# Performance work log

Hardware: AMD Instinct MI355X
Metric: run time of the kernel (lower is better)

The kernel has to match this reference:

```python
import jax, jax.numpy as jnp
import numpy as np

C_S = 384; C_Z = 128; C_RES = 128; H = 12; HD = 32; L = 8; RB = 2; NA = 7
TSF = 10.0; EPS = 1e-8; B = 2; N = 512; NRES = 21


def layernorm(x, g, b, eps=1e-5):
    m = jnp.mean(x, -1, keepdims=True)
    v = jnp.mean((x - m) ** 2, -1, keepdims=True)
    return (x - m) * jax.lax.rsqrt(v + eps) * g + b


def lin(x, w, b=None):
    y = x @ w.T
    return y if b is None else y + b


def rot_vec(R, v):
    return jnp.einsum('...ij,...j->...i', R, v)


def make_rigid(n, ca, c, eps=1e-7):
    # Gram-Schmidt backbone frame construction (openfold make_transform_from_reference)
    t = -ca
    n_xyz = n + t; c_xyz = c + t
    cx, cy, cz = c_xyz[..., 0], c_xyz[..., 1], c_xyz[..., 2]
    z = jnp.zeros_like(cx); o = jnp.ones_like(cx)
    nrm = jnp.sqrt(eps + cx**2 + cy**2)
    s1 = -cy / nrm; c1 = cx / nrm
    R1 = jnp.stack([jnp.stack([c1, -s1, z], -1), jnp.stack([s1, c1, z], -1), jnp.stack([z, z, o], -1)], -2)
    nrm2 = jnp.sqrt(eps + cx**2 + cy**2 + cz**2)
    s2 = cz / nrm2; c2 = jnp.sqrt(cx**2 + cy**2) / nrm2
    R2 = jnp.stack([jnp.stack([c2, z, s2], -1), jnp.stack([z, o, z], -1), jnp.stack([-s2, z, c2], -1)], -2)
    Rc = R2 @ R1
    n2 = rot_vec(Rc, n_xyz)
    ny, nz = n2[..., 1], n2[..., 2]
    nrm3 = jnp.sqrt(eps + ny**2 + nz**2)
    sn = -nz / nrm3; cn = ny / nrm3
    Rn = jnp.stack([jnp.stack([o, z, z], -1), jnp.stack([z, cn, -sn], -1), jnp.stack([z, sn, cn], -1)], -2)
    R = jnp.swapaxes(Rn @ Rc, -1, -2)
    return R, ca


def to4x4(R, t):
    bot = jnp.zeros(R.shape[:-2] + (1, 4), R.dtype).at[..., 0, 3].set(1.0)
    top = jnp.concatenate([R, t[..., None]], -1)
    return jnp.concatenate([top, bot], -2)


def compose(R1, t1, R2, t2):
    return R1 @ R2, rot_vec(R1, t2) + t1


def structure_fwd(s, z, aatype, mask, ln_s_g, ln_s_b, ln_z_g, ln_z_b, w_in, b_in, w_b, b_b,
                  attn_ln_g, attn_ln_b, attn_wqkv, attn_wo, attn_bo, attn_wg, attn_bg,
                  tr_ln_g, tr_ln_b, tr_w1, tr_b1, tr_w2, tr_b2, w_bb, b_bb,
                  ar_win, ar_bin, ar_winit, ar_binit, ar_w1, ar_b1, ar_w2, ar_b2, ar_wout, ar_bout,
                  default_frames, group_idx, atom_mask, lit_positions):
    Bd, Nd = s.shape[:2]
    s = layernorm(s, ln_s_g, ln_s_b)
    s_init = s
    s = lin(s, w_in, b_in)
    zn = layernorm(z, ln_z_g, ln_z_b)
    bmat = lin(zn, w_b, b_b)                                # [B,N,N,L*H]
    bmat = jnp.transpose(bmat, (0, 3, 1, 2)).reshape(Bd, L, H, Nd, Nd)
    key_mask = (mask[:, None, None, :] == 0)
    for i in range(L):
        xn = layernorm(s, attn_ln_g[i], attn_ln_b[i])
        t = lin(xn, attn_wqkv[i]).reshape(Bd, Nd, H, 3 * HD).transpose(0, 2, 1, 3)
        q, k, v = jnp.split(t, 3, axis=-1)                  # each [B,H,N,HD]
        a = jnp.einsum('bhqc,bhkc->bhqk', q * HD ** -0.5, k) + bmat[:, i]
        a = jnp.where(key_mask, -1e9, a)
        a = jax.nn.softmax(a, axis=-1)
        y = jnp.einsum('bhqk,bhkc->bqhc', a, v).reshape(Bd, Nd, C_S)
        g = jax.nn.sigmoid(lin(xn, attn_wg[i], attn_bg[i]))
        s = s + lin(g * y, attn_wo[i], attn_bo[i])
        xt = layernorm(s, tr_ln_g[i], tr_ln_b[i])
        s = s + lin(jax.nn.relu(lin(xt, tr_w1[i], tr_b1[i])), tr_w2[i], tr_b2[i])
    # angle resnet
    a0 = lin(jax.nn.relu(s_init), ar_winit, ar_binit)
    a = lin(jax.nn.relu(s), ar_win, ar_bin) + a0
    for j in range(RB):
        h = lin(jax.nn.relu(a), ar_w1[j], ar_b1[j])
        h = lin(jax.nn.relu(h), ar_w2[j], ar_b2[j])
        a = a + h
    ang = lin(jax.nn.relu(a), ar_wout, ar_bout).reshape(Bd, Nd, NA, 2)
    unnorm = ang
    denom = jnp.sqrt(jnp.maximum(jnp.sum(ang ** 2, -1, keepdims=True), EPS))
    angles = ang / denom
    # backbone rigid from predicted pseudo-atoms
    n_, ca_, c_ = jnp.split(lin(s, w_bb, b_bb), 3, axis=-1)
    Rbb, tbb = make_rigid(n_, ca_, c_)
    tbb = tbb * TSF
    # torsion_angles_to_frames
    d4 = default_frames[aatype]                             # [B,N,8,4,4]
    dR = d4[..., :3, :3]; dt = d4[..., :3, 3]
    bb_sin = jnp.zeros(angles.shape[:-2] + (1,), angles.dtype)
    bb_cos = jnp.ones_like(bb_sin)
    sin_a = jnp.concatenate([bb_sin, angles[..., 0]], -1)   # [B,N,8]
    cos_a = jnp.concatenate([bb_cos, angles[..., 1]], -1)
    z8 = jnp.zeros_like(sin_a); o8 = jnp.ones_like(sin_a)
    Ra = jnp.stack([jnp.stack([o8, z8, z8], -1), jnp.stack([z8, cos_a, -sin_a], -1), jnp.stack([z8, sin_a, cos_a], -1)], -2)
    Rf = dR @ Ra; tf = dt
    R5, t5 = compose(Rf[..., 4, :, :], tf[..., 4, :], Rf[..., 5, :, :], tf[..., 5, :])
    R6, t6 = compose(R5, t5, Rf[..., 6, :, :], tf[..., 6, :])
    R7, t7 = compose(R6, t6, Rf[..., 7, :, :], tf[..., 7, :])
    Rall = jnp.concatenate([Rf[..., :5, :, :], jnp.stack([R5, R6, R7], -3)], -3)
    tall = jnp.concatenate([tf[..., :5, :], jnp.stack([t5, t6, t7], -2)], -2)
    Rg = jnp.einsum('bnij,bngjk->bngik', Rbb, Rall)
    tg = jnp.einsum('bnij,bngj->bngi', Rbb, tall) + tbb[..., None, :]
    # frames + literature positions -> atom14
    oh = jax.nn.one_hot(group_idx[aatype], 8, dtype=Rg.dtype)   # [B,N,14,8]
    Ratom = jnp.einsum('bnag,bngij->bnaij', oh, Rg)
    tatom = jnp.einsum('bnag,bngi->bnai', oh, tg)
    lit = lit_positions[aatype]                             # [B,N,14,3]
    pred = jnp.einsum('bnaij,bnaj->bnai', Ratom, lit) + tatom
    pred = pred * atom_mask[aatype][..., None]
    return angles, unnorm, to4x4(Rbb, tbb), to4x4(Rg, tg), pred, s


def setup_inputs():
    key = jax.random.key(0)
    ks = iter(jax.random.split(key, 64))
    nrm = lambda shape: jax.random.normal(next(ks), shape, jnp.float32) * 0.02
    d = {}
    d['s'] = jax.random.normal(next(ks), (B, N, C_S), jnp.float32)
    d['z'] = jax.random.normal(next(ks), (B, N, N, C_Z), jnp.float32)
    d['aatype'] = jax.random.randint(next(ks), (B, N), 0, NRES)
    d['mask'] = jax.random.randint(next(ks), (B, N), 0, 2).astype(jnp.int32)
    d['ln_s_g'] = jnp.ones(C_S); d['ln_s_b'] = jnp.zeros(C_S)
    d['ln_z_g'] = jnp.ones(C_Z); d['ln_z_b'] = jnp.zeros(C_Z)
    d['w_in'] = nrm((C_S, C_S)); d['b_in'] = jnp.zeros(C_S)
    d['w_b'] = nrm((L * H, C_Z)); d['b_b'] = jnp.zeros(L * H)
    d['attn_ln_g'] = jnp.ones((L, C_S)); d['attn_ln_b'] = jnp.zeros((L, C_S))
    d['attn_wqkv'] = nrm((L, 3 * C_S, C_S))
    d['attn_wo'] = nrm((L, C_S, C_S)); d['attn_bo'] = jnp.zeros((L, C_S))
    d['attn_wg'] = nrm((L, C_S, C_S)); d['attn_bg'] = jnp.ones((L, C_S))
    d['tr_ln_g'] = jnp.ones((L, C_S)); d['tr_ln_b'] = jnp.zeros((L, C_S))
    d['tr_w1'] = nrm((L, C_S, C_S)); d['tr_b1'] = jnp.zeros((L, C_S))
    d['tr_w2'] = nrm((L, C_S, C_S)); d['tr_b2'] = jnp.zeros((L, C_S))
    d['w_bb'] = nrm((9, C_S)); d['b_bb'] = jnp.zeros(9)
    d['ar_win'] = nrm((C_RES, C_S)); d['ar_bin'] = jnp.zeros(C_RES)
    d['ar_winit'] = nrm((C_RES, C_S)); d['ar_binit'] = jnp.zeros(C_RES)
    d['ar_w1'] = nrm((RB, C_RES, C_RES)); d['ar_b1'] = jnp.zeros((RB, C_RES))
    d['ar_w2'] = nrm((RB, C_RES, C_RES)); d['ar_b2'] = jnp.zeros((RB, C_RES))
    d['ar_wout'] = nrm((2 * NA, C_RES)); d['ar_bout'] = jnp.zeros(2 * NA)
    df = jnp.tile(jnp.eye(4, dtype=jnp.float32), (NRES, 8, 1, 1))
    df = df.at[..., :3, 3].set(jax.random.normal(next(ks), (NRES, 8, 3)))
    d['default_frames'] = df
    d['group_idx'] = jax.random.randint(next(ks), (NRES, 14), 0, 8)
    d['atom_mask'] = (jax.random.uniform(next(ks), (NRES, 14)) < 0.9).astype(jnp.float32)
    d['lit_positions'] = jax.random.normal(next(ks), (NRES, 14, 3), jnp.float32)
    return d


def reference(s, z, aatype, mask, ln_s_g, ln_s_b, ln_z_g, ln_z_b, w_in, b_in, w_b, b_b,
              attn_ln_g, attn_ln_b, attn_wqkv, attn_wo, attn_bo, attn_wg, attn_bg,
              tr_ln_g, tr_ln_b, tr_w1, tr_b1, tr_w2, tr_b2, w_bb, b_bb,
              ar_win, ar_bin, ar_winit, ar_binit, ar_w1, ar_b1, ar_w2, ar_b2, ar_wout, ar_bout,
              default_frames, group_idx, atom_mask, lit_positions):
    return structure_fwd(s, z, aatype, mask, ln_s_g, ln_s_b, ln_z_g, ln_z_b, w_in, b_in, w_b, b_b,
                         attn_ln_g, attn_ln_b, attn_wqkv, attn_wo, attn_bo, attn_wg, attn_bg,
                         tr_ln_g, tr_ln_b, tr_w1, tr_b1, tr_w2, tr_b2, w_bb, b_bb,
                         ar_win, ar_bin, ar_winit, ar_binit, ar_w1, ar_b1, ar_w2, ar_b2, ar_wout, ar_bout,
                         default_frames, group_idx, atom_mask, lit_positions)
```

## Files before the change

### kernel.cpp

```cpp
#include <hip/hip_runtime.h>
#include <hip/hip_bf16.h>

typedef __attribute__((ext_vector_type(8))) short bf16x8;
typedef __attribute__((ext_vector_type(4))) float f32x4;
typedef unsigned short u16;

__device__ __forceinline__ u16 f2bf(float f) {
  union { __hip_bfloat16 b; u16 u; } v;
  v.b = __float2bfloat16(f);
  return v.u;
}
__device__ __forceinline__ float bf2f(u16 s) {
  union { unsigned u; float f; } v; v.u = ((unsigned)s) << 16;
  return v.f;
}
__device__ __forceinline__ f32x4 mfma_bf16(bf16x8 a, bf16x8 b, f32x4 c) {
  return __builtin_amdgcn_mfma_f32_16x16x32_bf16(a, b, c, 0, 0, 0);
}
__device__ __forceinline__ void split2(float x, u16& h, u16& l) {
  h = f2bf(x);
  l = f2bf(x - bf2f(h));
}
template <int SPL>
__device__ __forceinline__ void splitN(float x, u16* o) {
// ... 8 lines not shown
struct P2 { const float* s; u16* d; int n; };
struct Prep2Args { P2 j[7]; };
__global__ __launch_bounds__(256) void prep2_kernel(Prep2Args A, int total4) {
  for (int i4 = blockIdx.x * 256 + threadIdx.x; i4 < total4; i4 += gridDim.x * 256) {
    int i = i4 * 4;
    #pragma unroll
    for (int jj = 0; jj < 7; jj++) {
      if (i < A.j[jj].n) {
        const float* src = A.j[jj].s;
        u16* dh = A.j[jj].d;
        u16* dl = dh + A.j[jj].n;
        float4 v = *(const float4*)(src + i);
        ushort4 h, l;
        split2(v.x, h.x, l.x); split2(v.y, h.y, l.y);
        split2(v.z, h.z, l.z); split2(v.w, h.w, l.w);
        *(ushort4*)(dh + i) = h;
        *(ushort4*)(dl + i) = l;
        break;
      }
      i -= A.j[jj].n;
    }
  }
}
struct P3 { const float* s; u16* d; int n; };
struct Prep3Args { P3 j[4]; };
__global__ __launch_bounds__(256) void prep3_kernel(Prep3Args A, int total4) {
  for (int i4 = blockIdx.x * 256 + threadIdx.x; i4 < total4; i4 += gridDim.x * 256) {
    int i = i4 * 4;
    #pragma unroll
    for (int jj = 0; jj < 4; jj++) {
      if (i < A.j[jj].n) {
        const float* src = A.j[jj].s;
        u16* d0 = A.j[jj].d;
        u16* d1 = d0 + A.j[jj].n;
        u16* d2 = d1 + A.j[jj].n;
        float4 v = *(const float4*)(src + i);
        float xv[4] = {v.x, v.y, v.z, v.w};
        ushort4 o0, o1, o2;
        u16* po0 = (u16*)&o0; u16* po1 = (u16*)&o1; u16* po2 = (u16*)&o2;
        #pragma unroll
        for (int e = 0; e < 4; e++) {
          u16 tmp[3]; splitN<3>(xv[e], tmp);
          po0[e] = tmp[0]; po1[e] = tmp[1]; po2[e] = tmp[2];
        }
        *(ushort4*)(d0 + i) = o0;
        *(ushort4*)(d1 + i) = o1;
        *(ushort4*)(d2 + i) = o2;
        break;
      }
      i -= A.j[jj].n;
    }
  }
}

__global__ __launch_bounds__(256) void ln_kernel(
    const float* __restrict__ x, const float* __restrict__ gamma,
    const float* __restrict__ beta, float* __restrict__ o, int rows, int C) {
  int wid = threadIdx.x >> 6, lane = threadIdx.x & 63;
  int row = blockIdx.x * 4 + wid;
  if (row >= rows) return;
  const float* xr = x + (size_t)row * C;
  float s = 0.f, s2 = 0.f;
  for (int c = lane; c < C; c += 64) { float v = xr[c]; s += v; s2 += v * v; }
  #pragma unroll
  for (int off = 32; off >= 1; off >>= 1) {
    s += __shfl_xor(s, off);
    s2 += __shfl_xor(s2, off);
  }
  float m = s / C;
  float var = s2 / C - m * m;
  float rs = rsqrtf(var + 1e-5f);
  float* orow = o + (size_t)row * C;
  for (int c = lane; c < C; c += 64) orow[c] = (xr[c] - m) * rs * gamma[c] + beta[c];
}

template <int SPL, int LNA, int INRELU, int ACT, int ACC, int STATS, int OUT2>
__global__ __launch_bounds__(128) void gemm_kernel(
    const float* __restrict__ A, const float* __restrict__ pin,
    const float* __restrict__ lng, const float* __restrict__ lnb,
    const u16* __restrict__ w0p, const u16* __restrict__ w1p, const u16* __restrict__ w2p,
    const float* __restrict__ bias,
    float* __restrict__ O, float* __restrict__ O2, float* __restrict__ pout,
    int M, int N, int K) {
  __shared__ __align__(16) u16 a_pl[SPL][32][40];
  __shared__ __align__(16) u16 w_pl[SPL][64][40];
  const int n0 = blockIdx.x * 64, m0 = blockIdx.y * 32;
  const int t = threadIdx.x;
  const int wid = t >> 6, lane = t & 63;
  const int cl = lane & 15, cg = lane >> 4;
  const int ar = t >> 2, aq = t & 3;
  const int wr = t >> 1, wh2 = t & 1;
  const float* ap = A + (size_t)(m0 + ar) * K + aq * 8;
  const u16* wp[SPL];
  {
    const u16* tmp[3] = {w0p, w1p, w2p};
    #pragma unroll
    for (int p = 0; p < SPL; p++) wp[p] = tmp[p] + (size_t)(n0 + wr) * K + wh2 * 16;
  }
  float rm = 0.f, rrs = 1.f;
  if (LNA) {
    float s = 0.f, s2 = 0.f;
    #pragma unroll
    for (int pq = 0; pq < 6; pq++) {
      s  += pin[(m0 + ar) * 16 + pq * 2];
      s2 += pin[(m0 + ar) * 16 + pq * 2 + 1];
    }
    rm = s * (1.f / 384.f);
    rrs = rsqrtf(s2 * (1.f / 384.f) - rm * rm + 1e-5f);
  }
  float4 ra0, ra1, rg0, rg1, rb0, rb1;
  uint4 rw[SPL][2];
  auto GLOAD = [&](int k0) {
    ra0 = ((const float4*)(ap + k0))[0];
    ra1 = ((const float4*)(ap + k0))[1];
    #pragma unroll
    for (int p = 0; p < SPL; p++) {
      rw[p][0] = *(const uint4*)(wp[p] + k0);
      rw[p][1] = *(const uint4*)(wp[p] + k0 + 8);
    }
    if (LNA) {
      rg0 = ((const float4*)(lng + k0 + aq * 8))[0];
      rg1 = ((const float4*)(lng + k0 + aq * 8))[1];
      rb0 = ((const float4*)(lnb + k0 + aq * 8))[0];
      rb1 = ((const float4*)(lnb + k0 + aq * 8))[1];
    }
  };
  GLOAD(0);
  f32x4 acc[4] = {};
  for (int k0 = 0; k0 < K; k0 += 32) {
    {
      float av[8] = {ra0.x, ra0.y, ra0.z, ra0.w, ra1.x, ra1.y, ra1.z, ra1.w};
      if (LNA) {
        float gv[8] = {rg0.x, rg0.y, rg0.z, rg0.w, rg1.x, rg1.y, rg1.z, rg1.w};
        float bv[8] = {rb0.x, rb0.y, rb0.z, rb0.w, rb1.x, rb1.y, rb1.z, rb1.w};
        #pragma unroll
        for (int j = 0; j < 8; j++) av[j] = (av[j] - rm) * rrs * gv[j] + bv[j];
      }
      if (INRELU) {
        #pragma unroll
        for (int j = 0; j < 8; j++) av[j] = fmaxf(av[j], 0.f);
      }
      union { u16 s[8]; uint4 u; } pk[SPL];
      #pragma unroll
      for (int j = 0; j < 8; j++) {
        u16 tmp[SPL]; splitN<SPL>(av[j], tmp);
        #pragma unroll
        for (int p = 0; p < SPL; p++) pk[p].s[j] = tmp[p];
      }
      #pragma unroll
      for (int p = 0; p < SPL; p++) *(uint4*)&a_pl[p][ar][aq * 8] = pk[p].u;
      #pragma unroll
      for (int p = 0; p < SPL; p++) {
        *(uint4*)&w_pl[p][wr][wh2 * 16] = rw[p][0];
        *(uint4*)&w_pl[p][wr][wh2 * 16 + 8] = rw[p][1];
      }
    }
    __syncthreads();
    if (k0 + 32 < K) GLOAD(k0 + 32);
    bf16x8 av[SPL];
    #pragma unroll
    for (int p = 0; p < SPL; p++) av[p] = *(const bf16x8*)&a_pl[p][wid * 16 + cl][cg * 8];
    bf16x8 bv[SPL][4];
    #pragma unroll
    for (int p = 0; p < SPL; p++)
      #pragma unroll
      for (int nt = 0; nt < 4; nt++)
        bv[p][nt] = *(const bf16x8*)&w_pl[p][nt * 16 + cl][cg * 8];
    #pragma unroll
    for (int d = 0; d < SPL; d++)
      #pragma unroll
      for (int i2 = 0; i2 <= d; i2++) {
        #pragma unroll
        for (int nt = 0; nt < 4; nt++)
          acc[nt] = mfma_bf16(av[i2], bv[d - i2][nt], acc[nt]);
      }
    __syncthreads();
  }
  float ps[4], ps2[4];
  #pragma unroll
  for (int i = 0; i < 4; i++) { ps[i] = 0.f; ps2[i] = 0.f; }
  #pragma unroll
  for (int nt = 0; nt < 4; nt++) {
    #pragma unroll
    for (int i = 0; i < 4; i++) {
      int r = m0 + wid * 16 + cg * 4 + i;
      int c = n0 + nt * 16 + cl;
      float v = acc[nt][i];
      if (bias) v += bias[c];
      if (ACT == 1) v = fmaxf(v, 0.f);
      if (ACT == 2) v = 1.f / (1.f + __expf(-v));
      size_t oi = (size_t)r * N + c;
      float nv = ACC ? (O[oi] + v) : v;
      O[oi] = nv;
      if (OUT2) O2[oi] = nv;
      if (STATS) { ps[i] += nv; ps2[i] += nv * nv; }
    }
  }
  if (STATS) {
    #pragma unroll
    for (int i = 0; i < 4; i++) {
      #pragma unroll
      for (int off = 1; off < 16; off <<= 1) {
        ps[i] += __shfl_xor(ps[i], off);
        ps2[i] += __shfl_xor(ps2[i], off);
      }
    }
    if (cl == 0) {
      #pragma unroll
      for (int i = 0; i < 4; i++) {
        int r = m0 + wid * 16 + cg * 4 + i;
        pout[r * 16 + blockIdx.x * 2] = ps[i];
        pout[r * 16 + blockIdx.x * 2 + 1] = ps2[i];
      }
    }
  }
}

__global__ __launch_bounds__(128) void gemm_qkvg_kernel(
    const float* __restrict__ A, const float* __restrict__ pin,
    const float* __restrict__ lng, const float* __restrict__ lnb,
    const u16* __restrict__ wqh, const u16* __restrict__ wql,
    const u16* __restrict__ wgh, const u16* __restrict__ wgl,
    const float* __restrict__ bg,
    u16* __restrict__ qkvh, u16* __restrict__ qkvl, float* __restrict__ gbuf) {
  __shared__ __align__(16) u16 a_pl[2][32][40];
  __shared__ __align__(16) u16 w_pl[2][64][40];
  const int n0 = blockIdx.x * 64, m0 = blockIdx.y * 32;
  const bool isg = (n0 >= 1152);
  const int t = threadIdx.x;
  const int wid = t >> 6, lane = t & 63;
  const int cl = lane & 15, cg = lane >> 4;
  const int ar = t >> 2, aq = t & 3;
  const int wr = t >> 1, wh2 = t & 1;
  const float* ap = A + (size_t)(m0 + ar) * 384 + aq * 8;
  const u16* wph = (isg ? wgh + (size_t)(n0 - 1152 + wr) * 384 : wqh + (size_t)(n0 + wr) * 384) + wh2 * 16;
  const u16* wpl = (isg ? wgl + (size_t)(n0 - 1152 + wr) * 384 : wql + (size_t)(n0 + wr) * 384) + wh2 * 16;
  float s = 0.f, s2 = 0.f;
  #pragma unroll
  for (int pq = 0; pq < 6; pq++) {
    s  += pin[(m0 + ar) * 16 + pq * 2];
    s2 += pin[(m0 + ar) * 16 + pq * 2 + 1];
  }
  const float rm = s * (1.f / 384.f);
  const float rrs = rsqrtf(s2 * (1.f / 384.f) - rm * rm + 1e-5f);
  float4 ra0, ra1, rg0, rg1, rb0, rb1;
  uint4 rwh0, rwh1, rwl0, rwl1;
  auto GLOAD = [&](int k0) {
    ra0 = ((const float4*)(ap + k0))[0];
    ra1 = ((const float4*)(ap + k0))[1];
    rwh0 = *(const uint4*)(wph + k0);
    rwh1 = *(const uint4*)(wph + k0 + 8);
    rwl0 = *(const uint4*)(wpl + k0);
    rwl1 = *(const uint4*)(wpl + k0 + 8);
    rg0 = ((const float4*)(lng + k0 + aq * 8))[0];
    rg1 = ((const float4*)(lng + k0 + aq * 8))[1];
    rb0 = ((const float4*)(lnb + k0 + aq * 8))[0];
    rb1 = ((const float4*)(lnb + k0 + aq * 8))[1];
  };
  GLOAD(0);
  f32x4 acc[4] = {};
  for (int k0 = 0; k0 < 384; k0 += 32) {
    {
      float av[8] = {ra0.x, ra0.y, ra0.z, ra0.w, ra1.x, ra1.y, ra1.z, ra1.w};
      float gv[8] = {rg0.x, rg0.y, rg0.z, rg0.w, rg1.x, rg1.y, rg1.z, rg1.w};
      float bv[8] = {rb0.x, rb0.y, rb0.z, rb0.w, rb1.x, rb1.y, rb1.z, rb1.w};
      union { u16 s[8]; uint4 u; } ph, pl;
      #pragma unroll
      for (int j = 0; j < 8; j++) {
        float x = (av[j] - rm) * rrs * gv[j] + bv[j];
        split2(x, ph.s[j], pl.s[j]);
      }
      *(uint4*)&a_pl[0][ar][aq * 8] = ph.u;
      *(uint4*)&a_pl[1][ar][aq * 8] = pl.u;
      *(uint4*)&w_pl[0][wr][wh2 * 16] = rwh0;
      *(uint4*)&w_pl[0][wr][wh2 * 16 + 8] = rwh1;
      *(uint4*)&w_pl[1][wr][wh2 * 16] = rwl0;
      *(uint4*)&w_pl[1][wr][wh2 * 16 + 8] = rwl1;
    }
    __syncthreads();
    if (k0 + 32 < 384) GLOAD(k0 + 32);
    bf16x8 ah = *(const bf16x8*)&a_pl[0][wid * 16 + cl][cg * 8];
    bf16x8 al = *(const bf16x8*)&a_pl[1][wid * 16 + cl][cg * 8];
    bf16x8 bh[4], bl[4];
    #pragma unroll
    for (int nt = 0; nt < 4; nt++) {
      bh[nt] = *(const bf16x8*)&w_pl[0][nt * 16 + cl][cg * 8];
      bl[nt] = *(const bf16x8*)&w_pl[1][nt * 16 + cl][cg * 8];
    }
    #pragma unroll
    for (int nt = 0; nt < 4; nt++) acc[nt] = mfma_bf16(ah, bh[nt], acc[nt]);
    #pragma unroll
    for (int nt = 0; nt < 4; nt++) acc[nt] = mfma_bf16(ah, bl[nt], acc[nt]);
    #pragma unroll
    for (int nt = 0; nt < 4; nt++) acc[nt] = mfma_bf16(al, bh[nt], acc[nt]);
    __syncthreads();
  }
  #pragma unroll
  for (int nt = 0; nt < 4; nt++) {
    #pragma unroll
    for (int i = 0; i < 4; i++) {
      int r = m0 + wid * 16 + cg * 4 + i;
      int c = n0 + nt * 16 + cl;
      float v = acc[nt][i];
      if (isg) {
        int cc = c - 1152;
        v = 1.f / (1.f + __expf(-(v + bg[cc])));
        gbuf[(size_t)r * 384 + cc] = v;
      } else {
        u16 hh, ll; split2(v, hh, ll);
        qkvh[(size_t)r * 1152 + c] = hh;
        qkvl[(size_t)r * 1152 + c] = ll;
      }
    }
  }
}

__global__ __launch_bounds__(512) void zbmat_kernel(
    const float* __restrict__ z, const float* __restrict__ gamma,
    const float* __restrict__ beta, const u16* __restrict__ wbh,
    const u16* __restrict__ wbl, const float* __restrict__ bbias,
    float* __restrict__ bm) {
  __shared__ __align__(16) u16 w_h[96][136], w_l[96][136];
  __shared__ __align__(16) u16 a_h[2][64][136], a_l[2][64][136];
  const int b = blockIdx.x >> 9;
  const int i = blockIdx.x & 511;
  const int t = threadIdx.x;
  for (int idx = t; idx < 1536; idx += 512) {
    int r2 = idx >> 4, c2 = (idx & 15) * 8;
    *(uint4*)&w_h[r2][c2] = *(const uint4*)(wbh + r2 * 128 + c2);
    *(uint4*)&w_l[r2][c2] = *(const uint4*)(wbl + r2 * 128 + c2);
  }
  const int r = t >> 3, q = t & 7;
  const int cq = q * 16;
  const float* zbase = z + ((size_t)(b * 512 + i) * 512) * 128 + (size_t)r * 128 + cq;
  float4 gv[4], bv[4];
  #pragma unroll
  for (int ii = 0; ii < 4; ii++) {
    gv[ii] = *(const float4*)(gamma + cq + ii * 4);
    bv[ii] = *(const float4*)(beta + cq + ii * 4);
  }
  const int wid = t >> 6, lane = t & 63;
  const int cl = lane & 15, cg = lane >> 4;
  const int m = wid & 3, g = wid >> 2;
  const int arow = m * 16 + cl;
  float bb[3];
  #pragma unroll
  for (int nt = 0; nt < 3; nt++) bb[nt] = bbias[(g * 3 + nt) * 16 + cl];
  float4 v[4];

  auto ln_store = [&](int dst) {
    float s = 0.f, s2 = 0.f;
    #pragma unroll
    for (int ii = 0; ii < 4; ii++) {
      s += v[ii].x + v[ii].y + v[ii].z + v[ii].w;
      s2 += v[ii].x * v[ii].x + v[ii].y * v[ii].y + v[ii].z * v[ii].z + v[ii].w * v[ii].w;
    }
    s += __shfl_xor(s, 1); s2 += __shfl_xor(s2, 1);
    s += __shfl_xor(s, 2); s2 += __shfl_xor(s2, 2);
    s += __shfl_xor(s, 4); s2 += __shfl_xor(s2, 4);
    const float mu = s * (1.f / 128.f);
    const float var = s2 * (1.f / 128.f) - mu * mu;
    const float rs = rsqrtf(var + 1e-5f);
    float xv[16];
    #pragma unroll
    for (int w2 = 0; w2 < 4; w2++) {
      float4 x = v[w2], g2 = gv[w2], be = bv[w2];
      xv[w2 * 4 + 0] = (x.x - mu) * rs * g2.x + be.x;
      xv[w2 * 4 + 1] = (x.y - mu) * rs * g2.y + be.y;
      xv[w2 * 4 + 2] = (x.z - mu) * rs * g2.z + be.z;
      xv[w2 * 4 + 3] = (x.w - mu) * rs * g2.w + be.w;
    }
    union { u16 s[8]; uint4 u; } ph, pl;
    #pragma unroll
    for (int j = 0; j < 8; j++) split2(xv[j], ph.s[j], pl.s[j]);
    *(uint4*)&a_h[dst][r][cq] = ph.u;
    *(uint4*)&a_l[dst][r][cq] = pl.u;
    #pragma unroll
    for (int j = 0; j < 8; j++) split2(xv[8 + j], ph.s[j], pl.s[j]);
    *(uint4*)&a_h[dst][r][cq + 8] = ph.u;
    *(uint4*)&a_l[dst][r][cq + 8] = pl.u;
  };

  #pragma unroll
  for (int ii = 0; ii < 4; ii++) v[ii] = ((const float4*)zbase)[ii];
  ln_store(0);
  __syncthreads();

  int cur = 0;
  for (int jt = 0; jt < 8; jt++) {
    if (jt < 7) {
      const float* src = zbase + (size_t)(jt + 1) * 64 * 128;
      #pragma unroll
      for (int ii = 0; ii < 4; ii++) v[ii] = ((const float4*)src)[ii];
    }
    f32x4 acc[3] = {};
    #pragma unroll
    for (int ks = 0; ks < 4; ks++) {
      bf16x8 ah = *(const bf16x8*)&a_h[cur][arow][ks * 32 + cg * 8];
      bf16x8 al = *(const bf16x8*)&a_l[cur][arow][ks * 32 + cg * 8];
      bf16x8 bh[3], bl[3];
      #pragma unroll
      for (int nt = 0; nt < 3; nt++) {
        bh[nt] = *(const bf16x8*)&w_h[(g * 3 + nt) * 16 + cl][ks * 32 + cg * 8];
        bl[nt] = *(const bf16x8*)&w_l[(g * 3 + nt) * 16 + cl][ks * 32 + cg * 8];
      }
      #pragma unroll
      for (int nt = 0; nt < 3; nt++) acc[nt] = mfma_bf16(ah, bh[nt], acc[nt]);
      #pragma unroll
// ... 263 lines not shown
  tall[6][0] += tall[5][0]; tall[6][1] += tall[5][1]; tall[6][2] += tall[5][2];
  m3m(Rall[7], Rall[6], Rf[7]); m3v(tall[7], Rall[6], tf[7]);
  tall[7][0] += tall[6][0]; tall[7][1] += tall[6][1]; tall[7][2] += tall[6][2];
  float RG[8][9], TG[8][3];
  for (int g = 0; g < 8; g++) {
    m3m(RG[g], Rb, Rall[g]);
    m3v(TG[g], Rb, tall[g]);
    TG[g][0] += tb[0]; TG[g][1] += tb[1]; TG[g][2] += tb[2];
    float* o = o_rg4 + ((size_t)idx * 8 + g) * 16;
    o[0] = RG[g][0]; o[1] = RG[g][1]; o[2] = RG[g][2]; o[3] = TG[g][0];
    o[4] = RG[g][3]; o[5] = RG[g][4]; o[6] = RG[g][5]; o[7] = TG[g][1];
    o[8] = RG[g][6]; o[9] = RG[g][7]; o[10] = RG[g][8]; o[11] = TG[g][2];
    o[12] = 0.f; o[13] = 0.f; o[14] = 0.f; o[15] = 1.f;
  }
  for (int a = 0; a < 14; a++) {
    int gi = gidx[aa * 14 + a];
    const float* lp = lit + ((size_t)aa * 14 + a) * 3;
    float mk = amask[aa * 14 + a];
    float px = RG[gi][0] * lp[0] + RG[gi][1] * lp[1] + RG[gi][2] * lp[2] + TG[gi][0];
    float py = RG[gi][3] * lp[0] + RG[gi][4] * lp[1] + RG[gi][5] * lp[2] + TG[gi][1];
    float pz = RG[gi][6] * lp[0] + RG[gi][7] * lp[1] + RG[gi][8] * lp[2] + TG[gi][2];
    float* op = o_pred + ((size_t)idx * 14 + a) * 3;
    op[0] = px * mk; op[1] = py * mk; op[2] = pz * mk;
  }
}

extern "C" void kernel_launch(void* const* d_in, const int* in_sizes, int n_in,
                              void* d_out, int out_size, void* d_ws, size_t ws_size,
                              hipStream_t stream) {
  (void)in_sizes; (void)n_in; (void)out_size; (void)ws_size;
  const float* s_in    = (const float*)d_in[0];
  const float* z_in    = (const float*)d_in[1];
  const int*   aatype  = (const int*)d_in[2];
  const int*   maskp   = (const int*)d_in[3];
  const float* ln_s_g  = (const float*)d_in[4];
  const float* ln_s_b  = (const float*)d_in[5];
  const float* ln_z_g  = (const float*)d_in[6];
  const float* ln_z_b  = (const float*)d_in[7];
  const float* w_in    = (const float*)d_in[8];
  const float* b_in    = (const float*)d_in[9];
  const float* w_b     = (const float*)d_in[10];
  const float* b_b     = (const float*)d_in[11];
  const float* attn_ln_g = (const float*)d_in[12];
  const float* attn_ln_b = (const float*)d_in[13];
  const float* attn_wqkv = (const float*)d_in[14];
  const float* attn_wo   = (const float*)d_in[15];
  const float* attn_bo   = (const float*)d_in[16];
  const float* attn_wg   = (const float*)d_in[17];
  const float* attn_bg   = (const float*)d_in[18];
  const float* tr_ln_g   = (const float*)d_in[19];
  const float* tr_ln_b   = (const float*)d_in[20];
  const float* tr_w1     = (const float*)d_in[21];
  const float* tr_b1     = (const float*)d_in[22];
  const float* tr_w2     = (const float*)d_in[23];
  const float* tr_b2     = (const float*)d_in[24];
  const float* w_bb      = (const float*)d_in[25];
  const float* b_bb      = (const float*)d_in[26];
  const float* ar_win    = (const float*)d_in[27];
  const float* ar_bin    = (const float*)d_in[28];
  const float* ar_winit  = (const float*)d_in[29];
  const float* ar_binit  = (const float*)d_in[30];
  const float* ar_w1     = (const float*)d_in[31];
  const float* ar_b1     = (const float*)d_in[32];
  const float* ar_w2     = (const float*)d_in[33];
  const float* ar_b2     = (const float*)d_in[34];
  const float* ar_wout   = (const float*)d_in[35];
  const float* ar_bout   = (const float*)d_in[36];
  const float* def_frames= (const float*)d_in[37];
  const int*   group_idx = (const int*)d_in[38];
  const float* atom_mask = (const float*)d_in[39];
  const float* lit_pos   = (const float*)d_in[40];

  char* p = (char*)d_ws;
  float* bmat   = (float*)p;          p += 201326592;
  float* s_init = (float*)p;          p += 1572864;
  float* s_cur  = (float*)p;          p += 1572864;
  u16*   qkvh   = (u16*)p;            p += 2359296;
  u16*   qkvl   = (u16*)p;            p += 2359296;
  float* gbuf   = (float*)p;          p += 1572864;
  float* ybuf   = (float*)p;          p += 1572864;
  float* h1buf  = (float*)p;          p += 1572864;
  float* abuf   = (float*)p;          p += 524288;
  float* htmp   = (float*)p;          p += 524288;
  float* pbuf   = (float*)p;          p += 65536;
  float* bbbuf  = (float*)p;          p += 36864;
  float* angraw = (float*)p;          p += 57344;
  u16* ps_qkvw  = (u16*)p;            p += 14155776;
  u16* ps_wg    = (u16*)p;            p += 4718592;
  u16* ps_wo    = (u16*)p;            p += 4718592;
  u16* ps_tr1   = (u16*)p;            p += 4718592;
  u16* ps_tr2   = (u16*)p;            p += 4718592;
  u16* ps_win   = (u16*)p;            p += 589824;
  u16* ps_wb    = (u16*)p;            p += 49152;
  u16* ps_arwin = (u16*)p;            p += 294912;
  u16* ps_arwinit = (u16*)p;          p += 294912;
  u16* ps_arw1  = (u16*)p;            p += 196608;
  u16* ps_arw2  = (u16*)p;            p += 196608;

  float* out    = (float*)d_out;
  float* o_ang  = out;
  float* o_un   = out + 14336;
  float* o_bb4  = out + 28672;
  float* o_rg4  = out + 45056;
  float* o_pred = out + 176128;
  float* o_s    = out + 219136;

  Prep2Args p2;
  p2.j[0] = {attn_wqkv, ps_qkvw, 3538944};
  p2.j[1] = {attn_wg,   ps_wg,   1179648};
  p2.j[2] = {attn_wo,   ps_wo,   1179648};
  p2.j[3] = {tr_w1,     ps_tr1,  1179648};
  p2.j[4] = {tr_w2,     ps_tr2,  1179648};
  p2.j[5] = {w_in,      ps_win,  147456};
  p2.j[6] = {w_b,       ps_wb,   12288};
  prep2_kernel<<<2048, 256, 0, stream>>>(p2, 2104320);
  Prep3Args p3;
  p3.j[0] = {ar_win,   ps_arwin,   49152};
  p3.j[1] = {ar_winit, ps_arwinit, 49152};
  p3.j[2] = {ar_w1,    ps_arw1,    32768};
  p3.j[3] = {ar_w2,    ps_arw2,    32768};
  prep3_kernel<<<160, 256, 0, stream>>>(p3, 40960);

  ln_kernel<<<256, 256, 0, stream>>>(s_in, ln_s_g, ln_s_b, s_init, 1024, 384);
  gemm_kernel<2, 0, 0, 0, 0, 1, 0><<<dim3(6, 32), 128, 0, stream>>>(
      s_init, nullptr, nullptr, nullptr, ps_win, ps_win + 147456, nullptr,
      b_in, s_cur, nullptr, pbuf, 1024, 384, 384);
  zbmat_kernel<<<1024, 512, 0, stream>>>(z_in, ln_z_g, ln_z_b, ps_wb, ps_wb + 12288, b_b, bmat);

  for (int l = 0; l < 8; ++l) {
    gemm_qkvg_kernel<<<dim3(24, 32), 128, 0, stream>>>(
        s_cur, pbuf, attn_ln_g + l * 384, attn_ln_b + l * 384,
        ps_qkvw + (size_t)l * 442368, ps_qkvw + 3538944 + (size_t)l * 442368,
        ps_wg + (size_t)l * 147456, ps_wg + 1179648 + (size_t)l * 147456,
        attn_bg + l * 384, qkvh, qkvl, gbuf);
    attn_kernel<<<384, 128, 0, stream>>>(qkvh, qkvl, bmat, maskp, gbuf, ybuf, l);
    gemm_kernel<2, 0, 0, 0, 1, 1, 0><<<dim3(6, 32), 128, 0, stream>>>(
        ybuf, nullptr, nullptr, nullptr,
        ps_wo + (size_t)l * 147456, ps_wo + 1179648 + (size_t)l * 147456, nullptr,
        attn_bo + l * 384, s_cur, nullptr, pbuf, 1024, 384, 384);
    gemm_kernel<2, 1, 0, 1, 0, 0, 0><<<dim3(6, 32), 128, 0, stream>>>(
        s_cur, pbuf, tr_ln_g + l * 384, tr_ln_b + l * 384,
        ps_tr1 + (size_t)l * 147456, ps_tr1 + 1179648 + (size_t)l * 147456, nullptr,
        tr_b1 + l * 384, h1buf, nullptr, nullptr, 1024, 384, 384);
    if (l < 7)
      gemm_kernel<2, 0, 0, 0, 1, 1, 0><<<dim3(6, 32), 128, 0, stream>>>(
          h1buf, nullptr, nullptr, nullptr,
          ps_tr2 + (size_t)l * 147456, ps_tr2 + 1179648 + (size_t)l * 147456, nullptr,
          tr_b2 + l * 384, s_cur, nullptr, pbuf, 1024, 384, 384);
    else
      gemm_kernel<2, 0, 0, 0, 1, 1, 1><<<dim3(6, 32), 128, 0, stream>>>(
          h1buf, nullptr, nullptr, nullptr,
          ps_tr2 + (size_t)l * 147456, ps_tr2 + 1179648 + (size_t)l * 147456, nullptr,
          tr_b2 + l * 384, s_cur, o_s, pbuf, 1024, 384, 384);
  }

  gemm_kernel<3, 0, 1, 0, 0, 0, 0><<<dim3(2, 32), 128, 0, stream>>>(
      s_cur, nullptr, nullptr, nullptr,
      ps_arwin, ps_arwin + 49152, ps_arwin + 98304,
      ar_bin, abuf, nullptr, nullptr, 1024, 128, 384);
  gemm_kernel<3, 0, 1, 0, 1, 0, 0><<<dim3(2, 32), 128, 0, stream>>>(
      s_init, nullptr, nullptr, nullptr,
      ps_arwinit, ps_arwinit + 49152, ps_arwinit + 98304,
      ar_binit, abuf, nullptr, nullptr, 1024, 128, 384);
  for (int j = 0; j < 2; ++j) {
    gemm_kernel<3, 0, 1, 0, 0, 0, 0><<<dim3(2, 32), 128, 0, stream>>>(
        abuf, nullptr, nullptr, nullptr,
        ps_arw1 + j * 16384, ps_arw1 + 32768 + j * 16384, ps_arw1 + 65536 + j * 16384,
        ar_b1 + j * 128, htmp, nullptr, nullptr, 1024, 128, 128);
    gemm_kernel<3, 0, 1, 0, 1, 0, 0><<<dim3(2, 32), 128, 0, stream>>>(
        htmp, nullptr, nullptr, nullptr,
        ps_arw2 + j * 16384, ps_arw2 + 32768 + j * 16384, ps_arw2 + 65536 + j * 16384,
        ar_b2 + j * 128, abuf, nullptr, nullptr, 1024, 128, 128);
  }

  proj_kernel<9, 384, 0><<<256, 256, 0, stream>>>(s_cur, w_bb, b_bb, bbbuf);
  proj_kernel<14, 128, 1><<<256, 256, 0, stream>>>(abuf, ar_wout, ar_bout, angraw);
  tail_kernel<<<4, 256, 0, stream>>>(angraw, bbbuf, aatype, def_frames, group_idx,
                                     atom_mask, lit_pos, o_ang, o_un, o_bb4, o_rg4, o_pred);
}
```

Measured before the change: 1.098 ms.

## Retile split-bf16 GEMMs to 16x64 blocks with K-step 64 and per-wave column split

```diff
diff --git a/kernel.cpp b/kernel.cpp
--- a/kernel.cpp
+++ b/kernel.cpp
@@ -114,57 +114,56 @@
     const float* __restrict__ bias,
     float* __restrict__ O, float* __restrict__ O2, float* __restrict__ pout,
     int M, int N, int K) {
-  __shared__ __align__(16) u16 a_pl[SPL][32][40];
-  __shared__ __align__(16) u16 w_pl[SPL][64][40];
-  const int n0 = blockIdx.x * 64, m0 = blockIdx.y * 32;
+  __shared__ __align__(16) u16 a_pl[SPL][16][72];
+  __shared__ __align__(16) u16 w_pl[SPL][64][72];
+  const int n0 = blockIdx.x * 64, m0 = blockIdx.y * 16;
   const int t = threadIdx.x;
   const int wid = t >> 6, lane = t & 63;
   const int cl = lane & 15, cg = lane >> 4;
-  const int ar = t >> 2, aq = t & 3;
+  const int ar = t >> 3, aq = t & 7;
   const int wr = t >> 1, wh2 = t & 1;
   const float* ap = A + (size_t)(m0 + ar) * K + aq * 8;
-  const u16* wp[SPL];
+  const u16* wp[3] = {nullptr, nullptr, nullptr};
   {
     const u16* tmp[3] = {w0p, w1p, w2p};
     #pragma unroll
-    for (int p = 0; p < SPL; p++) wp[p] = tmp[p] + (size_t)(n0 + wr) * K + wh2 * 16;
+    for (int p = 0; p < SPL; p++) wp[p] = tmp[p] + (size_t)(n0 + wr) * K + wh2 * 32;
   }
   float rm = 0.f, rrs = 1.f;
   if (LNA) {
     float s = 0.f, s2 = 0.f;
     #pragma unroll
-    for (int pq = 0; pq < 6; pq++) {
-      s  += pin[(m0 + ar) * 16 + pq * 2];
-      s2 += pin[(m0 + ar) * 16 + pq * 2 + 1];
+    for (int pq = 0; pq < 12; pq++) {
+      s  += pin[(m0 + ar) * 32 + pq * 2];
+      s2 += pin[(m0 + ar) * 32 + pq * 2 + 1];
     }
     rm = s * (1.f / 384.f);
     rrs = rsqrtf(s2 * (1.f / 384.f) - rm * rm + 1e-5f);
   }
-  float4 ra0, ra1, rg0, rg1, rb0, rb1;
-  uint4 rw[SPL][2];
+  float4 ra[2], rg[2], rb4[2];
+  uint4 rw[SPL][4];
   auto GLOAD = [&](int k0) {
-    ra0 = ((const float4*)(ap + k0))[0];
-    ra1 = ((const float4*)(ap + k0))[1];
-    #pragma unroll
-    for (int p = 0; p < SPL; p++) {
-      rw[p][0] = *(const uint4*)(wp[p] + k0);
-      rw[p][1] = *(const uint4*)(wp[p] + k0 + 8);
-    }
+    ra[0] = ((const float4*)(ap + k0))[0];
+    ra[1] = ((const float4*)(ap + k0))[1];
+    #pragma unroll
+    for (int p = 0; p < SPL; p++)
+      #pragma unroll
+      for (int e = 0; e < 4; e++) rw[p][e] = *(const uint4*)(wp[p] + k0 + e * 8);
     if (LNA) {
-      rg0 = ((const float4*)(lng + k0 + aq * 8))[0];
-      rg1 = ((const float4*)(lng + k0 + aq * 8))[1];
-      rb0 = ((const float4*)(lnb + k0 + aq * 8))[0];
-      rb1 = ((const float4*)(lnb + k0 + aq * 8))[1];
+      rg[0]  = ((const float4*)(lng + k0 + aq * 8))[0];
+      rg[1]  = ((const float4*)(lng + k0 + aq * 8))[1];
+      rb4[0] = ((const float4*)(lnb + k0 + aq * 8))[0];
+      rb4[1] = ((const float4*)(lnb + k0 + aq * 8))[1];
     }
   };
   GLOAD(0);
-  f32x4 acc[4] = {};
-  for (int k0 = 0; k0 < K; k0 += 32) {
+  f32x4 acc[2] = {};
+  for (int k0 = 0; k0 < K; k0 += 64) {
     {
-      float av[8] = {ra0.x, ra0.y, ra0.z, ra0.w, ra1.x, ra1.y, ra1.z, ra1.w};
+      float av[8] = {ra[0].x, ra[0].y, ra[0].z, ra[0].w, ra[1].x, ra[1].y, ra[1].z, ra[1].w};
       if (LNA) {
-        float gv[8] = {rg0.x, rg0.y, rg0.z, rg0.w, rg1.x, rg1.y, rg1.z, rg1.w};
-        float bv[8] = {rb0.x, rb0.y, rb0.z, rb0.w, rb1.x, rb1.y, rb1.z, rb1.w};
+        float gv[8] = {rg[0].x, rg[0].y, rg[0].z, rg[0].w, rg[1].x, rg[1].y, rg[1].z, rg[1].w};
+        float bv[8] = {rb4[0].x, rb4[0].y, rb4[0].z, rb4[0].w, rb4[1].x, rb4[1].y, rb4[1].z, rb4[1].w};
         #pragma unroll
         for (int j = 0; j < 8; j++) av[j] = (av[j] - rm) * rrs * gv[j] + bv[j];
       }
@@ -172,52 +171,55 @@
         #pragma unroll
         for (int j = 0; j < 8; j++) av[j] = fmaxf(av[j], 0.f);
       }
-      union { u16 s[8]; uint4 u; } pk[SPL];
+      u16 sh[SPL][8];
       #pragma unroll
       for (int j = 0; j < 8; j++) {
         u16 tmp[SPL]; splitN<SPL>(av[j], tmp);
         #pragma unroll
-        for (int p = 0; p < SPL; p++) pk[p].s[j] = tmp[p];
-      }
-      #pragma unroll
-      for (int p = 0; p < SPL; p++) *(uint4*)&a_pl[p][ar][aq * 8] = pk[p].u;
+        for (int p = 0; p < SPL; p++) sh[p][j] = tmp[p];
+      }
       #pragma unroll
       for (int p = 0; p < SPL; p++) {
-        *(uint4*)&w_pl[p][wr][wh2 * 16] = rw[p][0];
-        *(uint4*)&w_pl[p][wr][wh2 * 16 + 8] = rw[p][1];
+        *(uint4*)&a_pl[p][ar][aq * 8] = *(const uint4*)&sh[p][0];
+        #pragma unroll
+        for (int e = 0; e < 4; e++) *(uint4*)&w_pl[p][wr][wh2 * 32 + e * 8] = rw[p][e];
       }
     }
     __syncthreads();
-    if (k0 + 32 < K) GLOAD(k0 + 32);
-    bf16x8 av[SPL];
-    #pragma unroll
-    for (int p = 0; p < SPL; p++) av[p] = *(const bf16x8*)&a_pl[p][wid * 16 + cl][cg * 8];
-    bf16x8 bv[SPL][4];
-    #pragma unroll
-    for (int p = 0; p < SPL; p++)
-      #pragma unroll
-      for (int nt = 0; nt < 4; nt++)
-        bv[p][nt] = *(const bf16x8*)&w_pl[p][nt * 16 + cl][cg * 8];
-    #pragma unroll
-    for (int d = 0; d < SPL; d++)
-      #pragma unroll
-      for (int i2 = 0; i2 <= d; i2++) {
+    if (k0 + 64 < K) GLOAD(k0 + 64);
+    #pragma unroll
+    for (int ks2 = 0; ks2 < 2; ks2++) {
+      bf16x8 av_[SPL];
+      #pragma unroll
+      for (int p = 0; p < SPL; p++)
+        av_[p] = *(const bf16x8*)&a_pl[p][cl][ks2 * 32 + cg * 8];
+      bf16x8 bv[SPL][2];
+      #pragma unroll
+      for (int p = 0; p < SPL; p++)
         #pragma unroll
-        for (int nt = 0; nt < 4; nt++)
-          acc[nt] = mfma_bf16(av[i2], bv[d - i2][nt], acc[nt]);
-      }
+        for (int ntl = 0; ntl < 2; ntl++)
+          bv[p][ntl] = *(const bf16x8*)&w_pl[p][(wid * 2 + ntl) * 16 + cl][ks2 * 32 + cg * 8];
+      #pragma unroll
+      for (int d = 0; d < SPL; d++)
+        #pragma unroll
+        for (int i2 = 0; i2 <= d; i2++) {
+          #pragma unroll
+          for (int ntl = 0; ntl < 2; ntl++)
+            acc[ntl] = mfma_bf16(av_[i2], bv[d - i2][ntl], acc[ntl]);
+        }
+    }
     __syncthreads();
   }
   float ps[4], ps2[4];
   #pragma unroll
   for (int i = 0; i < 4; i++) { ps[i] = 0.f; ps2[i] = 0.f; }
   #pragma unroll
-  for (int nt = 0; nt < 4; nt++) {
+  for (int ntl = 0; ntl < 2; ntl++) {
     #pragma unroll
     for (int i = 0; i < 4; i++) {
-      int r = m0 + wid * 16 + cg * 4 + i;
-      int c = n0 + nt * 16 + cl;
-      float v = acc[nt][i];
+      int r = m0 + cg * 4 + i;
+      int c = n0 + (wid * 2 + ntl) * 16 + cl;
+      float v = acc[ntl][i];
       if (bias) v += bias[c];
       if (ACT == 1) v = fmaxf(v, 0.f);
       if (ACT == 2) v = 1.f / (1.f + __expf(-v));
@@ -240,9 +242,9 @@
     if (cl == 0) {
       #pragma unroll
       for (int i = 0; i < 4; i++) {
-        int r = m0 + wid * 16 + cg * 4 + i;
-        pout[r * 16 + blockIdx.x * 2] = ps[i];
-        pout[r * 16 + blockIdx.x * 2 + 1] = ps2[i];
+        int r = m0 + cg * 4 + i;
+        pout[r * 32 + (blockIdx.x * 2 + wid) * 2] = ps[i];
+        pout[r * 32 + (blockIdx.x * 2 + wid) * 2 + 1] = ps2[i];
       }
     }
   }
@@ -255,85 +257,90 @@
     const u16* __restrict__ wgh, const u16* __restrict__ wgl,
     const float* __restrict__ bg,
     u16* __restrict__ qkvh, u16* __restrict__ qkvl, float* __restrict__ gbuf) {
-  __shared__ __align__(16) u16 a_pl[2][32][40];
-  __shared__ __align__(16) u16 w_pl[2][64][40];
-  const int n0 = blockIdx.x * 64, m0 = blockIdx.y * 32;
+  __shared__ __align__(16) u16 a_pl[2][16][72];
+  __shared__ __align__(16) u16 w_pl[2][64][72];
+  const int n0 = blockIdx.x * 64, m0 = blockIdx.y * 16;
   const bool isg = (n0 >= 1152);
   const int t = threadIdx.x;
   const int wid = t >> 6, lane = t & 63;
   const int cl = lane & 15, cg = lane >> 4;
-  const int ar = t >> 2, aq = t & 3;
+  const int ar = t >> 3, aq = t & 7;
   const int wr = t >> 1, wh2 = t & 1;
   const float* ap = A + (size_t)(m0 + ar) * 384 + aq * 8;
-  const u16* wph = (isg ? wgh + (size_t)(n0 - 1152 + wr) * 384 : wqh + (size_t)(n0 + wr) * 384) + wh2 * 16;
-  const u16* wpl = (isg ? wgl + (size_t)(n0 - 1152 + wr) * 384 : wql + (size_t)(n0 + wr) * 384) + wh2 * 16;
+  const u16* wph = (isg ? wgh + (size_t)(n0 - 1152 + wr) * 384 : wqh + (size_t)(n0 + wr) * 384) + wh2 * 32;
+  const u16* wpl = (isg ? wgl + (size_t)(n0 - 1152 + wr) * 384 : wql + (size_t)(n0 + wr) * 384) + wh2 * 32;
   float s = 0.f, s2 = 0.f;
   #pragma unroll
-  for (int pq = 0; pq < 6; pq++) {
-    s  += pin[(m0 + ar) * 16 + pq * 2];
-    s2 += pin[(m0 + ar) * 16 + pq * 2 + 1];
+  for (int pq = 0; pq < 12; pq++) {
+    s  += pin[(m0 + ar) * 32 + pq * 2];
+    s2 += pin[(m0 + ar) * 32 + pq * 2 + 1];
   }
   const float rm = s * (1.f / 384.f);
   const float rrs = rsqrtf(s2 * (1.f / 384.f) - rm * rm + 1e-5f);
-  float4 ra0, ra1, rg0, rg1, rb0, rb1;
-  uint4 rwh0, rwh1, rwl0, rwl1;
+  float4 ra[2], rg[2], rb4[2];
+  uint4 rwh[4], rwl[4];
   auto GLOAD = [&](int k0) {
-    ra0 = ((const float4*)(ap + k0))[0];
-    ra1 = ((const float4*)(ap + k0))[1];
-    rwh0 = *(const uint4*)(wph + k0);
-    rwh1 = *(const uint4*)(wph + k0 + 8);
-    rwl0 = *(const uint4*)(wpl + k0);
-    rwl1 = *(const uint4*)(wpl + k0 + 8);
-    rg0 = ((const float4*)(lng + k0 + aq * 8))[0];
-    rg1 = ((const float4*)(lng + k0 + aq * 8))[1];
-    rb0 = ((const float4*)(lnb + k0 + aq * 8))[0];
-    rb1 = ((const float4*)(lnb + k0 + aq * 8))[1];
+    ra[0] = ((const float4*)(ap + k0))[0];
+    ra[1] = ((const float4*)(ap + k0))[1];
+    #pragma unroll
+    for (int e = 0; e < 4; e++) {
+      rwh[e] = *(const uint4*)(wph + k0 + e * 8);
+      rwl[e] = *(const uint4*)(wpl + k0 + e * 8);
+    }
+    rg[0]  = ((const float4*)(lng + k0 + aq * 8))[0];
+    rg[1]  = ((const float4*)(lng + k0 + aq * 8))[1];
+    rb4[0] = ((const float4*)(lnb + k0 + aq * 8))[0];
+    rb4[1] = ((const float4*)(lnb + k0 + aq * 8))[1];
   };
   GLOAD(0);
-  f32x4 acc[4] = {};
-  for (int k0 = 0; k0 < 384; k0 += 32) {
+  f32x4 acc[2] = {};
+  for (int k0 = 0; k0 < 384; k0 += 64) {
     {
-      float av[8] = {ra0.x, ra0.y, ra0.z, ra0.w, ra1.x, ra1.y, ra1.z, ra1.w};
-      float gv[8] = {rg0.x, rg0.y, rg0.z, rg0.w, rg1.x, rg1.y, rg1.z, rg1.w};
-      float bv[8] = {rb0.x, rb0.y, rb0.z, rb0.w, rb1.x, rb1.y, rb1.z, rb1.w};
-      union { u16 s[8]; uint4 u; } ph, pl;
+      float av[8] = {ra[0].x, ra[0].y, ra[0].z, ra[0].w, ra[1].x, ra[1].y, ra[1].z, ra[1].w};
+      float gv[8] = {rg[0].x, rg[0].y, rg[0].z, rg[0].w, rg[1].x, rg[1].y, rg[1].z, rg[1].w};
+      float bv[8] = {rb4[0].x, rb4[0].y, rb4[0].z, rb4[0].w, rb4[1].x, rb4[1].y, rb4[1].z, rb4[1].w};
+      u16 sh[2][8];
       #pragma unroll
       for (int j = 0; j < 8; j++) {
         float x = (av[j] - rm) * rrs * gv[j] + bv[j];
-        split2(x, ph.s[j], pl.s[j]);
-      }
-      *(uint4*)&a_pl[0][ar][aq * 8] = ph.u;
-      *(uint4*)&a_pl[1][ar][aq * 8] = pl.u;
-      *(uint4*)&w_pl[0][wr][wh2 * 16] = rwh0;
-      *(uint4*)&w_pl[0][wr][wh2 * 16 + 8] = rwh1;
-      *(uint4*)&w_pl[1][wr][wh2 * 16] = rwl0;
-      *(uint4*)&w_pl[1][wr][wh2 * 16 + 8] = rwl1;
+        split2(x, sh[0][j], sh[1][j]);
+      }
+      #pragma unroll
+      for (int p = 0; p < 2; p++) *(uint4*)&a_pl[p][ar][aq * 8] = *(const uint4*)&sh[p][0];
+      #pragma unroll
+      for (int e = 0; e < 4; e++) {
+        *(uint4*)&w_pl[0][wr][wh2 * 32 + e * 8] = rwh[e];
+        *(uint4*)&w_pl[1][wr][wh2 * 32 + e * 8] = rwl[e];
+      }
     }
     __syncthreads();
-    if (k0 + 32 < 384) GLOAD(k0 + 32);
-    bf16x8 ah = *(const bf16x8*)&a_pl[0][wid * 16 + cl][cg * 8];
-    bf16x8 al = *(const bf16x8*)&a_pl[1][wid * 16 + cl][cg * 8];
-    bf16x8 bh[4], bl[4];
-    #pragma unroll
-    for (int nt = 0; nt < 4; nt++) {
-      bh[nt] = *(const bf16x8*)&w_pl[0][nt * 16 + cl][cg * 8];
-      bl[nt] = *(const bf16x8*)&w_pl[1][nt * 16 + cl][cg * 8];
-    }
-    #pragma unroll
-    for (int nt = 0; nt < 4; nt++) acc[nt] = mfma_bf16(ah, bh[nt], acc[nt]);
-    #pragma unroll
-    for (int nt = 0; nt < 4; nt++) acc[nt] = mfma_bf16(ah, bl[nt], acc[nt]);
-    #pragma unroll
-    for (int nt = 0; nt < 4; nt++) acc[nt] = mfma_bf16(al, bh[nt], acc[nt]);
+    if (k0 + 64 < 384) GLOAD(k0 + 64);
+    #pragma unroll
+    for (int ks2 = 0; ks2 < 2; ks2++) {
+      bf16x8 ah = *(const bf16x8*)&a_pl[0][cl][ks2 * 32 + cg * 8];
+      bf16x8 al = *(const bf16x8*)&a_pl[1][cl][ks2 * 32 + cg * 8];
+      bf16x8 bh[2], bl[2];
+      #pragma unroll
+      for (int ntl = 0; ntl < 2; ntl++) {
+        bh[ntl] = *(const bf16x8*)&w_pl[0][(wid * 2 + ntl) * 16 + cl][ks2 * 32 + cg * 8];
+        bl[ntl] = *(const bf16x8*)&w_pl[1][(wid * 2 + ntl) * 16 + cl][ks2 * 32 + cg * 8];
+      }
+      #pragma unroll
+      for (int ntl = 0; ntl < 2; ntl++) {
+        acc[ntl] = mfma_bf16(ah, bh[ntl], acc[ntl]);
+        acc[ntl] = mfma_bf16(ah, bl[ntl], acc[ntl]);
+        acc[ntl] = mfma_bf16(al, bh[ntl], acc[ntl]);
+      }
+    }
     __syncthreads();
   }
   #pragma unroll
-  for (int nt = 0; nt < 4; nt++) {
+  for (int ntl = 0; ntl < 2; ntl++) {
     #pragma unroll
     for (int i = 0; i < 4; i++) {
-      int r = m0 + wid * 16 + cg * 4 + i;
-      int c = n0 + nt * 16 + cl;
-      float v = acc[nt][i];
+      int r = m0 + cg * 4 + i;
+      int c = n0 + (wid * 2 + ntl) * 16 + cl;
+      float v = acc[ntl][i];
       if (isg) {
         int cc = c - 1152;
         v = 1.f / (1.f + __expf(-(v + bg[cc])));
@@ -354,8 +361,7 @@
     float* __restrict__ bm) {
   __shared__ __align__(16) u16 w_h[96][136], w_l[96][136];
   __shared__ __align__(16) u16 a_h[2][64][136], a_l[2][64][136];
-  const int b = blockIdx.x >> 9;
-  const int i = blockIdx.x & 511;
+  const int b = blockIdx.x >> 9, i = blockIdx.x & 511;
   const int t = threadIdx.x;
   for (int idx = t; idx < 1536; idx += 512) {
     int r2 = idx >> 4, c2 = (idx & 15) * 8;
@@ -785,8 +791,8 @@
   float* h1buf  = (float*)p;          p += 1572864;
   float* abuf   = (float*)p;          p += 524288;
   float* htmp   = (float*)p;          p += 524288;
-  float* pbuf   = (float*)p;          p += 65536;
-  float* bbbuf  = (float*)p;          p += 36864;
+  float* pbuf   = (float*)p;          p += 131072;
+  float* bbbuf  = (float*)p;          p += 65536;
   float* angraw = (float*)p;          p += 57344;
   u16* ps_qkvw  = (u16*)p;            p += 14155776;
   u16* ps_wg    = (u16*)p;            p += 4718592;
@@ -825,52 +831,52 @@
   prep3_kernel<<<160, 256, 0, stream>>>(p3, 40960);
 
   ln_kernel<<<256, 256, 0, stream>>>(s_in, ln_s_g, ln_s_b, s_init, 1024, 384);
-  gemm_kernel<2, 0, 0, 0, 0, 1, 0><<<dim3(6, 32), 128, 0, stream>>>(
+  gemm_kernel<2, 0, 0, 0, 0, 1, 0><<<dim3(6, 64), 128, 0, stream>>>(
       s_init, nullptr, nullptr, nullptr, ps_win, ps_win + 147456, nullptr,
       b_in, s_cur, nullptr, pbuf, 1024, 384, 384);
   zbmat_kernel<<<1024, 512, 0, stream>>>(z_in, ln_z_g, ln_z_b, ps_wb, ps_wb + 12288, b_b, bmat);
 
   for (int l = 0; l < 8; ++l) {
-    gemm_qkvg_kernel<<<dim3(24, 32), 128, 0, stream>>>(
+    gemm_qkvg_kernel<<<dim3(24, 64), 128, 0, stream>>>(
         s_cur, pbuf, attn_ln_g + l * 384, attn_ln_b + l * 384,
         ps_qkvw + (size_t)l * 442368, ps_qkvw + 3538944 + (size_t)l * 442368,
         ps_wg + (size_t)l * 147456, ps_wg + 1179648 + (size_t)l * 147456,
         attn_bg + l * 384, qkvh, qkvl, gbuf);
     attn_kernel<<<384, 128, 0, stream>>>(qkvh, qkvl, bmat, maskp, gbuf, ybuf, l);
-    gemm_kernel<2, 0, 0, 0, 1, 1, 0><<<dim3(6, 32), 128, 0, stream>>>(
+    gemm_kernel<2, 0, 0, 0, 1, 1, 0><<<dim3(6, 64), 128, 0, stream>>>(
         ybuf, nullptr, nullptr, nullptr,
         ps_wo + (size_t)l * 147456, ps_wo + 1179648 + (size_t)l * 147456, nullptr,
         attn_bo + l * 384, s_cur, nullptr, pbuf, 1024, 384, 384);
-    gemm_kernel<2, 1, 0, 1, 0, 0, 0><<<dim3(6, 32), 128, 0, stream>>>(
+    gemm_kernel<2, 1, 0, 1, 0, 0, 0><<<dim3(6, 64), 128, 0, stream>>>(
         s_cur, pbuf, tr_ln_g + l * 384, tr_ln_b + l * 384,
         ps_tr1 + (size_t)l * 147456, ps_tr1 + 1179648 + (size_t)l * 147456, nullptr,
         tr_b1 + l * 384, h1buf, nullptr, nullptr, 1024, 384, 384);
     if (l < 7)
-      gemm_kernel<2, 0, 0, 0, 1, 1, 0><<<dim3(6, 32), 128, 0, stream>>>(
+      gemm_kernel<2, 0, 0, 0, 1, 1, 0><<<dim3(6, 64), 128, 0, stream>>>(
           h1buf, nullptr, nullptr, nullptr,
           ps_tr2 + (size_t)l * 147456, ps_tr2 + 1179648 + (size_t)l * 147456, nullptr,
           tr_b2 + l * 384, s_cur, nullptr, pbuf, 1024, 384, 384);
     else
-      gemm_kernel<2, 0, 0, 0, 1, 1, 1><<<dim3(6, 32), 128, 0, stream>>>(
+      gemm_kernel<2, 0, 0, 0, 1, 1, 1><<<dim3(6, 64), 128, 0, stream>>>(
           h1buf, nullptr, nullptr, nullptr,
           ps_tr2 + (size_t)l * 147456, ps_tr2 + 1179648 + (size_t)l * 147456, nullptr,
           tr_b2 + l * 384, s_cur, o_s, pbuf, 1024, 384, 384);
   }
 
-  gemm_kernel<3, 0, 1, 0, 0, 0, 0><<<dim3(2, 32), 128, 0, stream>>>(
+  gemm_kernel<3, 0, 1, 0, 0, 0, 0><<<dim3(2, 64), 128, 0, stream>>>(
       s_cur, nullptr, nullptr, nullptr,
       ps_arwin, ps_arwin + 49152, ps_arwin + 98304,
       ar_bin, abuf, nullptr, nullptr, 1024, 128, 384);
-  gemm_kernel<3, 0, 1, 0, 1, 0, 0><<<dim3(2, 32), 128, 0, stream>>>(
+  gemm_kernel<3, 0, 1, 0, 1, 0, 0><<<dim3(2, 64), 128, 0, stream>>>(
       s_init, nullptr, nullptr, nullptr,
       ps_arwinit, ps_arwinit + 49152, ps_arwinit + 98304,
       ar_binit, abuf, nullptr, nullptr, 1024, 128, 384);
   for (int j = 0; j < 2; ++j) {
-    gemm_kernel<3, 0, 1, 0, 0, 0, 0><<<dim3(2, 32), 128, 0, stream>>>(
+    gemm_kernel<3, 0, 1, 0, 0, 0, 0><<<dim3(2, 64), 128, 0, stream>>>(
         abuf, nullptr, nullptr, nullptr,
         ps_arw1 + j * 16384, ps_arw1 + 32768 + j * 16384, ps_arw1 + 65536 + j * 16384,
         ar_b1 + j * 128, htmp, nullptr, nullptr, 1024, 128, 128);
-    gemm_kernel<3, 0, 1, 0, 1, 0, 0><<<dim3(2, 32), 128, 0, stream>>>(
+    gemm_kernel<3, 0, 1, 0, 1, 0, 0><<<dim3(2, 64), 128, 0, stream>>>(
         htmp, nullptr, nullptr, nullptr,
         ps_arw2 + j * 16384, ps_arw2 + 32768 + j * 16384, ps_arw2 + 65536 + j * 16384,
         ar_b2 + j * 128, abuf, nullptr, nullptr, 1024, 128, 128);
```

After: 1.369 ms. +24.6%, slower.
